# Optimization experiments

Measured on AMD Instinct MI355X. Metric: run time of the kernel, lower is better.

The kernel has to match this reference:

```python
import jax, jax.numpy as jnp
import numpy as np

B = 8192      # batch (num nodes)
D = 256       # embedding dim
K = 8         # positives per node -> nnz = B*K
EPS = 1e-8


def setup_inputs() -> dict:
    key = jax.random.key(0)
    k_emb, k_val = jax.random.split(key)
    embeddings = jax.random.normal(k_emb, (B, D), dtype=jnp.float32)
    # structured sparse positive mask: node i is positive with (i+1..i+K) mod B
    # -> unique pairs, row-major sorted (coalesced), no self loops
    rows = jnp.repeat(jnp.arange(B, dtype=jnp.int64), K)           # [B*K]
    offs = jnp.tile(jnp.arange(1, K + 1, dtype=jnp.int64), B)      # [B*K]
    cols = (rows + offs) % B
    pos_vals = jax.random.uniform(k_val, (B * K,), dtype=jnp.float32)
    temperature = jnp.float32(0.5)  # learnable scalar nn.Parameter
    return {
        "embeddings": embeddings,
        "pos_vals": pos_vals,
        "temperature": temperature,
        "pos_row": rows,
        "pos_col": cols,
    }


def reference(embeddings, pos_vals, temperature, pos_row, pos_col):
    n = embeddings.shape[0]
    # F.normalize(p=2, dim=1) with eps=1e-12
    norm = jnp.linalg.norm(embeddings, axis=1, keepdims=True)
    z = embeddings / jnp.maximum(norm, 1e-12)

    temp = jax.nn.softplus(temperature)
    sim = jnp.matmul(z, z.T) / temp                                 # [B,B]
    sim = sim - jax.lax.stop_gradient(jnp.max(sim, axis=1, keepdims=True))

    pos_dense = jnp.zeros((n, n), dtype=bool).at[pos_row, pos_col].set(True)
    identity = jnp.eye(n, dtype=bool)
    neg_mask = (~pos_dense) & (~identity)

    # pos weights: 'inverse_sim' -> 1 - values, min-max normalized
    pos_w = 1.0 - pos_vals
    pos_w = (pos_w - jnp.min(pos_w)) / (jnp.max(pos_w) - jnp.min(pos_w) + EPS)

    # neg weights: 'inverse_sim' -> min-max over negative sims, +1; weight_mat=1 elsewhere
    neg_min = jnp.min(jnp.where(neg_mask, sim, jnp.inf))
    neg_max = jnp.max(jnp.where(neg_mask, sim, -jnp.inf))
    neg_w = (sim - neg_min) / (neg_max - neg_min + EPS) + 1.0
    log_weight = jnp.where(neg_mask, jnp.log(neg_w), 0.0)

    log_probs = sim - jax.nn.logsumexp(sim + log_weight, axis=1, keepdims=True)

    pos_log = log_probs[pos_row, pos_col]   # same ordering as torch boolean index (coalesced mask)
    loss = -jnp.mean(pos_log * pos_w)
    return loss
```

## Files before the change

### kernel.cpp

```cpp
#include <hip/hip_runtime.h>

#define NB 8192
#define ND 256
#define NMASK 8191
#define CEPS 1e-8f
#define L2E 1.4426950408889634f
#define LN2 0.6931471805599453f

#if __has_builtin(__builtin_amdgcn_exp2f)
#define EXP2(x) __builtin_amdgcn_exp2f(x)
#else
#define EXP2(x) exp2f(x)
#endif

typedef float f32x4 __attribute__((ext_vector_type(4)));
typedef _Float16 half8 __attribute__((ext_vector_type(8)));
typedef _Float16 half4 __attribute__((ext_vector_type(4)));


__global__ void k_norm(const float* __restrict__ emb, const float* __restrict__ temperature,
                       const float* __restrict__ pos_vals, _Float16* __restrict__ zb,
                       float* __restrict__ bpvmin, float* __restrict__ bpvmax,
                       float* __restrict__ out) {
  const int tid = threadIdx.x, lane = tid & 63, w = tid >> 6;
  const int bid = blockIdx.x;
  if (bid == 0 && tid == 0) out[0] = 0.f;
  float sp = log1pf(expf(temperature[0]));
  float alpha = sqrtf(L2E / sp);
  int row = bid * 4 + w;
  const float4 e = *(const float4*)(emb + row * ND + lane * 4);
  float ss = e.x * e.x + e.y * e.y + e.z * e.z + e.w * e.w;
#pragma unroll
  for (int mk = 1; mk < 64; mk <<= 1) ss += __shfl_xor(ss, mk, 64);
  float rn = alpha / fmaxf(sqrtf(ss), 1e-12f);
  half4 h = {(_Float16)(e.x * rn), (_Float16)(e.y * rn),
             (_Float16)(e.z * rn), (_Float16)(e.w * rn)};
  *(half4*)(zb + row * ND + lane * 4) = h;
  if (w == 0) {
    float v = (lane < 32) ? pos_vals[bid * 32 + lane] : 0.f;
    float mn = (lane < 32) ? v : INFINITY;
    float mx = (lane < 32) ? v : -INFINITY;
#pragma unroll
    for (int mk = 1; mk < 32; mk <<= 1) {
      mn = fminf(mn, __shfl_xor(mn, mk, 64));
      mx = fmaxf(mx, __shfl_xor(mx, mk, 64));
    }
    if (lane == 0) { bpvmin[bid] = mn; bpvmax[bid] = mx; }
  }
}

__global__ __launch_bounds__(256) void k_gemm(
    const _Float16* __restrict__ zb, float2* __restrict__ EpR, float2* __restrict__ EpC,
    float* __restrict__ sBand, float* __restrict__ bmin, float* __restrict__ bmax) {
  __shared__ __align__(16) char smem[32768];
  const int tid = threadIdx.x, lane = tid & 63, w = tid >> 6;
  const int l15 = lane & 15, lq = lane >> 4;
  const int bid = blockIdx.x;
  int d, rb;
  if (bid < 2048) { d = bid >> 6; rb = bid & 63; }
  else { d = 32; rb = bid - 2048; }
  const int cb = (rb + d) & 63;
  const int roww = rb * 128 + w * 32;
  const int colbase = cb * 128;

  half8 aF[2][8];
#pragma unroll
  for (int mt = 0; mt < 2; ++mt)
#pragma unroll
    for (int kc = 0; kc < 8; ++kc)
      aF[mt][kc] = *(const half8*)(zb + (roww + mt * 16 + l15) * ND + kc * 32 + lq * 8);

  float E1r[8], Ear[8];
#pragma unroll
  for (int i = 0; i < 8; ++i) { E1r[i] = 0.f; Ear[i] = 0.f; }
  float2 cA[4][2];
#pragma unroll
  for (int s = 0; s < 4; ++s) { cA[s][0] = make_float2(0.f, 0.f); cA[s][1] = make_float2(0.f, 0.f); }
  float vmn = INFINITY, vmx = -INFINITY;

  const char* gsrc[4];
#pragma unroll
  for (int i = 0; i < 4; ++i) {
    int t = w * 4 + i, nt = t >> 3, kc = t & 7;
    gsrc[i] = (const char*)(zb + (colbase + nt * 16 + l15) * ND + kc * 32 + lq * 8);
  }
#pragma unroll
  for (int i = 0; i < 4; ++i)
    __builtin_amdgcn_global_load_lds(
        (const __attribute__((address_space(1))) void*)(gsrc[i]),
        (__attribute__((address_space(3))) void*)(smem + (w * 4 + i) * 1024), 16, 0, 0);

#pragma unroll
  for (int step = 0; step < 4; ++step) {
    __syncthreads();
    if (step < 3) {
      char* ld = smem + ((step + 1) & 1) * 16384;
#pragma unroll
      for (int i = 0; i < 4; ++i)
        __builtin_amdgcn_global_load_lds(
            (const __attribute__((address_space(1))) void*)(gsrc[i] + (step + 1) * 16384),
            (__attribute__((address_space(3))) void*)(ld + (w * 4 + i) * 1024), 16, 0, 0);
    }
    const char* buf = smem + (step & 1) * 16384;
    f32x4 acc[2][2];
#pragma unroll
    for (int mt = 0; mt < 2; ++mt) {
      acc[mt][0] = (f32x4){0.f, 0.f, 0.f, 0.f};
      acc[mt][1] = (f32x4){0.f, 0.f, 0.f, 0.f};
    }
#pragma unroll
    for (int kc = 0; kc < 8; ++kc) {
      half8 b0 = *(const half8*)(buf + kc * 1024 + lane * 16);
      half8 b1 = *(const half8*)(buf + (8 + kc) * 1024 + lane * 16);
#pragma unroll
      for (int mt = 0; mt < 2; ++mt) {
        acc[mt][0] = __builtin_amdgcn_mfma_f32_16x16x32_f16(aF[mt][kc], b0, acc[mt][0], 0, 0, 0);
        acc[mt][1] = __builtin_amdgcn_mfma_f32_16x16x32_f16(aF[mt][kc], b1, acc[mt][1], 0, 0, 0);
      }
    }
    const int offbase = (colbase + step * 32 + l15) - (roww + lq * 4);
    if (d >= 2) {
#pragma unroll
      for (int mt = 0; mt < 2; ++mt)
#pragma unroll
        for (int nt = 0; nt < 2; ++nt)
#pragma unroll
          for (int reg = 0; reg < 4; ++reg) {
            float t = acc[mt][nt][reg];
            float e = EXP2(t);
            E1r[mt * 4 + reg] += e;
            Ear[mt * 4 + reg] = fmaf(e, t, Ear[mt * 4 + reg]);
            cA[step][nt].x += e;
            cA[step][nt].y = fmaf(e, t, cA[step][nt].y);
            vmn = fminf(vmn, t);
            vmx = fmaxf(vmx, t);
          }
    } else if (d == 1) {
#pragma unroll
      for (int mt = 0; mt < 2; ++mt)
#pragma unroll
        for (int nt = 0; nt < 2; ++nt)
#pragma unroll
          for (int reg = 0; reg < 4; ++reg) {
            float t = acc[mt][nt][reg];
            float e = EXP2(t);
            E1r[mt * 4 + reg] += e;
            Ear[mt * 4 + reg] = fmaf(e, t, Ear[mt * 4 + reg]);
            cA[step][nt].x += e;
            cA[step][nt].y = fmaf(e, t, cA[step][nt].y);
            vmn = fminf(vmn, t);
            vmx = fmaxf(vmx, t);
            int off = (offbase + (nt - mt) * 16 - reg) & NMASK;
            if (off <= 8)
              sBand[(roww + mt * 16 + lq * 4 + reg) * 12 + off] = t;
          }
    } else {
#pragma unroll
      for (int mt = 0; mt < 2; ++mt)
#pragma unroll
        for (int nt = 0; nt < 2; ++nt)
#pragma unroll
          for (int reg = 0; reg < 4; ++reg) {
            float t = acc[mt][nt][reg];
            float e = EXP2(t);
            E1r[mt * 4 + reg] += e;
            Ear[mt * 4 + reg] = fmaf(e, t, Ear[mt * 4 + reg]);
            int off = (offbase + (nt - mt) * 16 - reg) & NMASK;
            bool isB = off <= 8;
            vmn = fminf(vmn, isB ? vmn : t);
            vmx = fmaxf(vmx, isB ? vmx : t);
            if (isB)
              sBand[(roww + mt * 16 + lq * 4 + reg) * 12 + off] = t;
          }
    }
  }

#pragma unroll
  for (int mk = 1; mk < 16; mk <<= 1)
#pragma unroll
    for (int i = 0; i < 8; ++i) {
      E1r[i] += __shfl_xor(E1r[i], mk, 64);
      Ear[i] += __shfl_xor(Ear[i], mk, 64);
    }
  if (l15 == 0) {
#pragma unroll
    for (int mt = 0; mt < 2; ++mt)
#pragma unroll
      for (int reg = 0; reg < 4; ++reg) {
        int row = roww + mt * 16 + lq * 4 + reg;
        EpR[d * NB + row] = make_float2(E1r[mt * 4 + reg], Ear[mt * 4 + reg]);
      }
  }
#pragma unroll
  for (int mk = 16; mk < 64; mk <<= 1)
#pragma unroll
    for (int s = 0; s < 4; ++s)
#pragma unroll
      for (int nt = 0; nt < 2; ++nt) {
        cA[s][nt].x += __shfl_xor(cA[s][nt].x, mk, 64);
        cA[s][nt].y += __shfl_xor(cA[s][nt].y, mk, 64);
      }
#pragma unroll
  for (int mk = 1; mk < 64; mk <<= 1) {
    vmn = fminf(vmn, __shfl_xor(vmn, mk, 64));
    vmx = fmaxf(vmx, __shfl_xor(vmx, mk, 64));
  }
  __syncthreads();
  float2* colAcc = (float2*)smem;
  float* redmm = (float*)(smem + 4096);
  if (d != 0 && lq == 0) {
#pragma unroll
    for (int s = 0; s < 4; ++s)
#pragma unroll
      for (int nt = 0; nt < 2; ++nt)
        colAcc[w * 128 + s * 32 + nt * 16 + l15] = cA[s][nt];
  }
  if (lane == 0) { redmm[w] = vmn; redmm[4 + w] = vmx; }
  __syncthreads();
  if (d != 0 && tid < 128) {
    float2 a = colAcc[tid], b = colAcc[128 + tid], c = colAcc[256 + tid], e = colAcc[384 + tid];
    EpC[d * NB + colbase + tid] = make_float2(a.x + b.x + c.x + e.x, a.y + b.y + c.y + e.y);
  }
  if (tid == 0) {
    bmin[bid] = fminf(fminf(redmm[0], redmm[1]), fminf(redmm[2], redmm[3]));
    bmax[bid] = fmaxf(fmaxf(redmm[4], redmm[5]), fmaxf(redmm[6], redmm[7]));
  }
}

__global__ void k_final(const float* __restrict__ pos_vals,
                        const float2* __restrict__ EpR, const float2* __restrict__ EpC,
                        const float* __restrict__ sBand,
                        const float* __restrict__ bmin, const float* __restrict__ bmax,
                        const float* __restrict__ bpvmin, const float* __restrict__ bpvmax,
                        float* __restrict__ out) {
  const int tid = threadIdx.x, lane = tid & 63, w = tid >> 6;
  __shared__ float sv[16];
  __shared__ float coef[4];
  float mn = INFINITY, mx = -INFINITY, pmn = INFINITY, pmx = -INFINITY;
  for (int i = tid; i < 2080; i += 256) { mn = fminf(mn, bmin[i]); mx = fmaxf(mx, bmax[i]); }
  for (int i = tid; i < 2048; i += 256) { pmn = fminf(pmn, bpvmin[i]); pmx = fmaxf(pmx, bpvmax[i]); }
#pragma unroll
  for (int mk = 1; mk < 64; mk <<= 1) {
    mn = fminf(mn, __shfl_xor(mn, mk, 64));
    mx = fmaxf(mx, __shfl_xor(mx, mk, 64));
    pmn = fminf(pmn, __shfl_xor(pmn, mk, 64));
    pmx = fmaxf(pmx, __shfl_xor(pmx, mk, 64));
  }
  if (lane == 0) { sv[w] = mn; sv[4 + w] = mx; sv[8 + w] = pmn; sv[12 + w] = pmx; }
  __syncthreads();
  if (tid == 0) {
    float tmin = fminf(fminf(sv[0], sv[1]), fminf(sv[2], sv[3]));
    float tmax = fmaxf(fmaxf(sv[4], sv[5]), fmaxf(sv[6], sv[7]));
    float pvmin = fminf(fminf(sv[8], sv[9]), fminf(sv[10], sv[11]));
    float pvmax = fmaxf(fmaxf(sv[12], sv[13]), fmaxf(sv[14], sv[15]));
    float At = LN2 / ((tmax - tmin) * LN2 + CEPS);
    coef[0] = At;
    coef[1] = 1.f - At * tmin;
    coef[2] = pvmax;
    coef[3] = 1.f / (pvmax - pvmin + CEPS);
  }
  __syncthreads();
  const float At = coef[0], Bt = coef[1], pvmax = coef[2], pwInv = coef[3];

  int row = blockIdx.x * 256 + tid;
  float e1 = 0.f, ea = 0.f;
#pragma unroll
  for (int dd = 0; dd < 32; ++dd) { float2 p = EpR[dd * NB + row]; e1 += p.x; ea += p.y; }
#pragma unroll
  for (int dd = 1; dd < 32; ++dd) { float2 p = EpC[dd * NB + row]; e1 += p.x; ea += p.y; }
  {
    float2 p = (row < 4096) ? EpR[32 * NB + row] : EpC[32 * NB + row];
    e1 += p.x; ea += p.y;
  }
  float tb[9], Sb = 0.f, Sbt = 0.f;
#pragma unroll
  for (int o = 0; o <= 8; ++o) {
    tb[o] = sBand[row * 12 + o];
    float e = EXP2(tb[o]);
    Sb += e;
    Sbt = fmaf(e, tb[o], Sbt);
  }
  float denom = At * (ea - Sbt) + Bt * (e1 - Sb) + Sb;
  float lse = logf(denom);
  float contrib = 0.f;
#pragma unroll
  for (int k = 0; k < 8; ++k) {
    float v = pos_vals[row * 8 + k];
    contrib += (pvmax - v) * pwInv * (tb[k + 1] * LN2 - lse);
  }
#pragma unroll
  for (int mk = 1; mk < 64; mk <<= 1) contrib += __shfl_xor(contrib, mk, 64);
  __syncthreads();
  if (lane == 0) sv[w] = contrib;
  __syncthreads();
  if (tid == 0)
    atomicAdd(out, -(sv[0] + sv[1] + sv[2] + sv[3]) * (1.0f / 65536.0f));
}

extern "C" void kernel_launch(void* const* d_in, const int* in_sizes, int n_in,
                              void* d_out, int out_size, void* d_ws, size_t ws_size,
                              hipStream_t stream) {
  const float* emb = (const float*)d_in[0];
  const float* pos_vals = (const float*)d_in[1];
  const float* temperature = (const float*)d_in[2];
  float* out = (float*)d_out;

  char* ws = (char*)d_ws;
  size_t off = 0;
  float2* EpR = (float2*)(ws + off); off += (size_t)33 * NB * 8;
  float2* EpC = (float2*)(ws + off); off += (size_t)33 * NB * 8;
  float* sBand = (float*)(ws + off); off += (size_t)NB * 12 * 4;
  float* bmin = (float*)(ws + off); off += 2080 * 4 + 128;
  float* bmax = (float*)(ws + off); off += 2080 * 4 + 128;
  float* bpvmin = (float*)(ws + off); off += 2048 * 4;
  float* bpvmax = (float*)(ws + off); off += 2048 * 4;
  _Float16* zb = (_Float16*)(ws + off); off += (size_t)NB * ND * 2;

  k_norm<<<2048, 256, 0, stream>>>(emb, temperature, pos_vals, zb, bpvmin, bpvmax, out);
  k_gemm<<<2080, 256, 0, stream>>>(zb, EpR, EpC, sBand, bmin, bmax);
  k_final<<<32, 256, 0, stream>>>(pos_vals, EpR, EpC, sBand, bmin, bmax, bpvmin, bpvmax, out);
}
```

Before: 117.4 us.

## Switch Gram-matrix GEMM from FP16 to FP8 with scaled MFMA

Normalized embeddings are now quantized to FP8 (e4m3) instead of FP16, and the GEMM uses the gfx950 scaled 16x16x128 f8f6f4 MFMA with unit scales. This halves the bytes loaded per tile, halves the LDS buffer, and cuts the MFMA instruction count by processing K=128 per instruction. The cost is reduced precision in the similarity logits, which feed exp and a min/max; FP8 rounding error on values scaled by sqrt(log2e/temp) may push the loss beyond tolerance.

```diff
diff --git a/kernel.cpp b/kernel.cpp
--- a/kernel.cpp
+++ b/kernel.cpp
@@ -6,6 +6,7 @@
 #define CEPS 1e-8f
 #define L2E 1.4426950408889634f
 #define LN2 0.6931471805599453f
+#define SC1 0x7F7F7F7F
 
 #if __has_builtin(__builtin_amdgcn_exp2f)
 #define EXP2(x) __builtin_amdgcn_exp2f(x)
@@ -14,12 +15,13 @@
 #endif
 
 typedef float f32x4 __attribute__((ext_vector_type(4)));
-typedef _Float16 half8 __attribute__((ext_vector_type(8)));
-typedef _Float16 half4 __attribute__((ext_vector_type(4)));
+typedef int v8i __attribute__((ext_vector_type(8)));
+typedef int v4i __attribute__((ext_vector_type(4)));
+union V8 { v8i v; v4i q[2]; };
 
 
 __global__ void k_norm(const float* __restrict__ emb, const float* __restrict__ temperature,
-                       const float* __restrict__ pos_vals, _Float16* __restrict__ zb,
+                       const float* __restrict__ pos_vals, char* __restrict__ zb8,
                        float* __restrict__ bpvmin, float* __restrict__ bpvmax,
                        float* __restrict__ out) {
   const int tid = threadIdx.x, lane = tid & 63, w = tid >> 6;
@@ -33,9 +35,9 @@
 #pragma unroll
   for (int mk = 1; mk < 64; mk <<= 1) ss += __shfl_xor(ss, mk, 64);
   float rn = alpha / fmaxf(sqrtf(ss), 1e-12f);
-  half4 h = {(_Float16)(e.x * rn), (_Float16)(e.y * rn),
-             (_Float16)(e.z * rn), (_Float16)(e.w * rn)};
-  *(half4*)(zb + row * ND + lane * 4) = h;
+  int pk = __builtin_amdgcn_cvt_pk_fp8_f32(e.x * rn, e.y * rn, 0, 0);
+  pk = __builtin_amdgcn_cvt_pk_fp8_f32(e.z * rn, e.w * rn, pk, 1);
+  *(int*)(zb8 + row * 256 + lane * 4) = pk;
   if (w == 0) {
     float v = (lane < 32) ? pos_vals[bid * 32 + lane] : 0.f;
     float mn = (lane < 32) ? v : INFINITY;
@@ -50,9 +52,9 @@
 }
 
 __global__ __launch_bounds__(256) void k_gemm(
-    const _Float16* __restrict__ zb, float2* __restrict__ EpR, float2* __restrict__ EpC,
+    const char* __restrict__ zb8, float2* __restrict__ EpR, float2* __restrict__ EpC,
     float* __restrict__ sBand, float* __restrict__ bmin, float* __restrict__ bmax) {
-  __shared__ __align__(16) char smem[32768];
+  __shared__ __align__(16) char smem[16384];
   const int tid = threadIdx.x, lane = tid & 63, w = tid >> 6;
   const int l15 = lane & 15, lq = lane >> 4;
   const int bid = blockIdx.x;
@@ -63,12 +65,16 @@
   const int roww = rb * 128 + w * 32;
   const int colbase = cb * 128;
 
-  half8 aF[2][8];
-#pragma unroll
-  for (int mt = 0; mt < 2; ++mt)
-#pragma unroll
-    for (int kc = 0; kc < 8; ++kc)
-      aF[mt][kc] = *(const half8*)(zb + (roww + mt * 16 + l15) * ND + kc * 32 + lq * 8);
+  V8 aF[2][2];
+#pragma unroll
+  for (int mt = 0; mt < 2; ++mt) {
+    const char* ar = zb8 + (roww + mt * 16 + l15) * 256 + lq * 32;
+#pragma unroll
+    for (int kc = 0; kc < 2; ++kc) {
+      aF[mt][kc].q[0] = *(const v4i*)(ar + kc * 128);
+      aF[mt][kc].q[1] = *(const v4i*)(ar + kc * 128 + 16);
+    }
+  }
 
   float E1r[8], Ear[8];
 #pragma unroll
@@ -78,30 +84,30 @@
   for (int s = 0; s < 4; ++s) { cA[s][0] = make_float2(0.f, 0.f); cA[s][1] = make_float2(0.f, 0.f); }
   float vmn = INFINITY, vmx = -INFINITY;
 
-  const char* gsrc[4];
-#pragma unroll
-  for (int i = 0; i < 4; ++i) {
-    int t = w * 4 + i, nt = t >> 3, kc = t & 7;
-    gsrc[i] = (const char*)(zb + (colbase + nt * 16 + l15) * ND + kc * 32 + lq * 8);
-  }
-#pragma unroll
-  for (int i = 0; i < 4; ++i)
+  const char* gsrc[2];
+#pragma unroll
+  for (int i = 0; i < 2; ++i) {
+    int j = w * 2 + i, T = j >> 1, h = j & 1, nt = T & 1, kc = T >> 1;
+    gsrc[i] = zb8 + (colbase + nt * 16 + l15) * 256 + kc * 128 + lq * 32 + h * 16;
+  }
+#pragma unroll
+  for (int i = 0; i < 2; ++i)
     __builtin_amdgcn_global_load_lds(
         (const __attribute__((address_space(1))) void*)(gsrc[i]),
-        (__attribute__((address_space(3))) void*)(smem + (w * 4 + i) * 1024), 16, 0, 0);
+        (__attribute__((address_space(3))) void*)(smem + (w * 2 + i) * 1024), 16, 0, 0);
 
 #pragma unroll
   for (int step = 0; step < 4; ++step) {
     __syncthreads();
     if (step < 3) {
-      char* ld = smem + ((step + 1) & 1) * 16384;
-#pragma unroll
-      for (int i = 0; i < 4; ++i)
+      char* ld = smem + ((step + 1) & 1) * 8192;
+#pragma unroll
+      for (int i = 0; i < 2; ++i)
         __builtin_amdgcn_global_load_lds(
-            (const __attribute__((address_space(1))) void*)(gsrc[i] + (step + 1) * 16384),
-            (__attribute__((address_space(3))) void*)(ld + (w * 4 + i) * 1024), 16, 0, 0);
-    }
-    const char* buf = smem + (step & 1) * 16384;
+            (const __attribute__((address_space(1))) void*)(gsrc[i] + (step + 1) * 8192),
+            (__attribute__((address_space(3))) void*)(ld + (w * 2 + i) * 1024), 16, 0, 0);
+    }
+    const char* buf = smem + (step & 1) * 8192;
     f32x4 acc[2][2];
 #pragma unroll
     for (int mt = 0; mt < 2; ++mt) {
@@ -109,13 +115,18 @@
       acc[mt][1] = (f32x4){0.f, 0.f, 0.f, 0.f};
     }
 #pragma unroll
-    for (int kc = 0; kc < 8; ++kc) {
-      half8 b0 = *(const half8*)(buf + kc * 1024 + lane * 16);
-      half8 b1 = *(const half8*)(buf + (8 + kc) * 1024 + lane * 16);
+    for (int kc = 0; kc < 2; ++kc) {
+      V8 b0, b1;
+      b0.q[0] = *(const v4i*)(buf + (kc * 2 + 0) * 2048 + lane * 16);
+      b0.q[1] = *(const v4i*)(buf + (kc * 2 + 0) * 2048 + 1024 + lane * 16);
+      b1.q[0] = *(const v4i*)(buf + (kc * 2 + 1) * 2048 + lane * 16);
+      b1.q[1] = *(const v4i*)(buf + (kc * 2 + 1) * 2048 + 1024 + lane * 16);
 #pragma unroll
       for (int mt = 0; mt < 2; ++mt) {
-        acc[mt][0] = __builtin_amdgcn_mfma_f32_16x16x32_f16(aF[mt][kc], b0, acc[mt][0], 0, 0, 0);
-        acc[mt][1] = __builtin_amdgcn_mfma_f32_16x16x32_f16(aF[mt][kc], b1, acc[mt][1], 0, 0, 0);
+        acc[mt][0] = __builtin_amdgcn_mfma_scale_f32_16x16x128_f8f6f4(
+            aF[mt][kc].v, b0.v, acc[mt][0], 0, 0, 0, SC1, 0, SC1);
+        acc[mt][1] = __builtin_amdgcn_mfma_scale_f32_16x16x128_f8f6f4(
+            aF[mt][kc].v, b1.v, acc[mt][1], 0, 0, 0, SC1, 0, SC1);
       }
     }
     const int offbase = (colbase + step * 32 + l15) - (roww + lq * 4);
@@ -314,9 +325,9 @@
   float* bmax = (float*)(ws + off); off += 2080 * 4 + 128;
   float* bpvmin = (float*)(ws + off); off += 2048 * 4;
   float* bpvmax = (float*)(ws + off); off += 2048 * 4;
-  _Float16* zb = (_Float16*)(ws + off); off += (size_t)NB * ND * 2;
-
-  k_norm<<<2048, 256, 0, stream>>>(emb, temperature, pos_vals, zb, bpvmin, bpvmax, out);
-  k_gemm<<<2080, 256, 0, stream>>>(zb, EpR, EpC, sBand, bmin, bmax);
+  char* zb8 = (char*)(ws + off); off += (size_t)NB * 256;
+
+  k_norm<<<2048, 256, 0, stream>>>(emb, temperature, pos_vals, zb8, bpvmin, bpvmax, out);
+  k_gemm<<<2080, 256, 0, stream>>>(zb8, EpR, EpC, sBand, bmin, bmax);
   k_final<<<32, 256, 0, stream>>>(pos_vals, EpR, EpC, sBand, bmin, bmax, bpvmin, bpvmax, out);
 }
```

Result: faster. 103.4 us (-11.9%).
